# Kernel tuning notes

Hardware: AMD Instinct MI355X
Metric: run time of the kernel (lower is better)

The kernel has to match this reference:

```python
import jax, jax.numpy as jnp
import numpy as np

NUM_HEADS = 12
WINDOW = 14  # window size == input_size[0]; rel pos tables are (2*WINDOW-1, head_dim)


def setup_inputs() -> dict:
    key = jax.random.key(0)
    ks = jax.random.split(key, 6)
    C = 768
    x = jax.random.normal(ks[0], (16, 56, 56, C), dtype=jnp.float32)
    qkv_w = jax.random.normal(ks[1], (3 * C, C), dtype=jnp.float32) * 0.02
    qkv_b = jnp.zeros((3 * C,), dtype=jnp.float32)
    proj_w = jax.random.normal(ks[2], (C, C), dtype=jnp.float32) * 0.02
    proj_b = jnp.zeros((C,), dtype=jnp.float32)
    hd = C // NUM_HEADS
    rel_pos_h = jax.random.normal(ks[3], (2 * WINDOW - 1, hd), dtype=jnp.float32) * 0.02
    rel_pos_w = jax.random.normal(ks[4], (2 * WINDOW - 1, hd), dtype=jnp.float32) * 0.02
    return {"x": x, "qkv_w": qkv_w, "qkv_b": qkv_b, "proj_w": proj_w,
            "proj_b": proj_b, "rel_pos_h": rel_pos_h, "rel_pos_w": rel_pos_w}


def reference(x, qkv_w, qkv_b, proj_w, proj_b, rel_pos_h, rel_pos_w):
    B, H, W, C = x.shape
    nh, ws = NUM_HEADS, WINDOW
    hd = C // nh
    scale = hd ** -0.5
    # --- window_partition (H, W divisible by ws -> no padding branch) ---
    xw = x.reshape(B, H // ws, ws, W // ws, ws, C)
    xw = xw.transpose(0, 1, 3, 2, 4, 5).reshape(-1, ws * ws, C)  # (Bw, N, C)
    Bw, N, _ = xw.shape
    # --- qkv projection ---
    qkv = xw @ qkv_w.T + qkv_b  # (Bw, N, 3C)
    qkv = qkv.reshape(Bw, N, 3, nh, hd).transpose(2, 0, 3, 1, 4)
    qkv = qkv.reshape(3, Bw * nh, N, hd)
    q, k, v = qkv[0], qkv[1], qkv[2]
    # --- scaled attention scores ---
    attn = jnp.einsum('bqd,bkd->bqk', q * scale, k)  # (Bw*nh, N, N)
    # --- decomposed relative position bias (q_size == k_size == ws) ---
    idx = jnp.arange(ws)[:, None] - jnp.arange(ws)[None, :] + (ws - 1)
    Rh = rel_pos_h[idx]  # (ws, ws, hd)
    Rw = rel_pos_w[idx]  # (ws, ws, hd)
    rq = q.reshape(Bw * nh, ws, ws, hd)
    rel_h = jnp.einsum('bhwc,hkc->bhwk', rq, Rh)
    rel_w = jnp.einsum('bhwc,wkc->bhwk', rq, Rw)
    attn = (attn.reshape(Bw * nh, ws, ws, ws, ws)
            + rel_h[:, :, :, :, None] + rel_w[:, :, :, None, :])
    attn = jax.nn.softmax(attn.reshape(Bw * nh, N, N), axis=-1)
    # --- weighted values + output projection ---
    out = jnp.einsum('bqk,bkd->bqd', attn, v)
    out = out.reshape(Bw, nh, ws, ws, hd).transpose(0, 2, 3, 1, 4).reshape(Bw, ws, ws, C)
    out = out @ proj_w.T + proj_b
    # --- window_unpartition ---
    out = out.reshape(B, H // ws, W // ws, ws, ws, C)
    out = out.transpose(0, 1, 3, 2, 4, 5).reshape(B, H, W, C)
    return out
```

## Files before the change

kernel.cpp:

```cpp
#include <hip/hip_runtime.h>
#include <stdint.h>

typedef __bf16 bfv8 __attribute__((ext_vector_type(8)));
typedef short s16x8 __attribute__((ext_vector_type(8)));
typedef short s16x4 __attribute__((ext_vector_type(4)));
typedef float f32x4 __attribute__((ext_vector_type(4)));
typedef float f32x16 __attribute__((ext_vector_type(16)));

#define MFMA(a, b, c) __builtin_amdgcn_mfma_f32_16x16x32_bf16(a, b, c, 0, 0, 0)
#define MFMA32(a, b, c) __builtin_amdgcn_mfma_f32_32x32x16_bf16(a, b, c, 0, 0, 0)

__device__ __forceinline__ short f2bf(float f) {
  union { float f; unsigned u; } v; v.f = f;
  unsigned r = v.u + 0x7FFFu + ((v.u >> 16) & 1u);
  return (short)(r >> 16);
}
__device__ __forceinline__ float bf2f(short s) {
  union { unsigned u; float f; } v; v.u = ((unsigned)(unsigned short)s) << 16;
  return v.f;
}
__device__ __forceinline__ unsigned pack2(float a, float b) {
  return (unsigned)(unsigned short)f2bf(a) | ((unsigned)(unsigned short)f2bf(b) << 16);
}
__device__ __forceinline__ bfv8 mkfrag(unsigned a, unsigned b, unsigned c, unsigned d) {
  union { unsigned u[4]; bfv8 v; } t; t.u[0] = a; t.u[1] = b; t.u[2] = c; t.u[3] = d;
  return t.v;
}

__device__ __forceinline__ void async_cp16(const short* g, short* l) {
  auto gp = reinterpret_cast<const uint32_t __attribute__((address_space(1)))*>(
      reinterpret_cast<uintptr_t>(g));
  auto lp = reinterpret_cast<uint32_t __attribute__((address_space(3)))*>(
      reinterpret_cast<uintptr_t>(l));
  __builtin_amdgcn_global_load_lds(gp, lp, 16, 0, 0);
}

__global__ __launch_bounds__(256) void convert_all(
    const float* __restrict__ x, const float* __restrict__ qkvw,
    const float* __restrict__ projw, const float* __restrict__ rph,
    const float* __restrict__ rpw, short* __restrict__ Xbf,
    short* __restrict__ Wq, short* __restrict__ Wp, short* __restrict__ Rhb,
    short* __restrict__ Rwb) {
  const int NX = 9633792;
  const int NW1 = 442368;
  const int NW2 = 147456;
  const int NR = 512;
  int idx = blockIdx.x * 256 + threadIdx.x;
  if (idx < NX) {
    int t = idx / 192, cq = idx - t * 192;
    int wdx = t / 196, n = t - wdx * 196;
    int b = wdx >> 4, wl = wdx & 15;
    int nh = n / 14;
    int hh = (wl >> 2) * 14 + nh;
    int ww = (wl & 3) * 14 + (n - nh * 14);
    float4 v = *(const float4*)(x + ((b * 56 + hh) * 56 + ww) * 768 + cq * 4);
    s16x4 s = {f2bf(v.x), f2bf(v.y), f2bf(v.z), f2bf(v.w)};
    *(s16x4*)(Xbf + idx * 4) = s;
  } else if (idx < NX + NW1) {
    int i = idx - NX;
    float4 v = ((const float4*)qkvw)[i];
    s16x4 s = {f2bf(v.x), f2bf(v.y), f2bf(v.z), f2bf(v.w)};
    *(s16x4*)(Wq + i * 4) = s;
  } else if (idx < NX + NW1 + NW2) {
    int i = idx - NX - NW1;
    float4 v = ((const float4*)projw)[i];
    s16x4 s = {f2bf(v.x), f2bf(v.y), f2bf(v.z), f2bf(v.w)};
    *(s16x4*)(Wp + i * 4) = s;
  } else if (idx < NX + NW1 + NW2 + 2 * NR) {
    int i = idx - NX - NW1 - NW2;
    int which = i >> 9;
    int j = i & 511;
    int p = j >> 4, q = j & 15;
    const float* src = which ? rpw : rph;
    short* dst = which ? Rwb : Rhb;
    s16x4 s = {0, 0, 0, 0};
    if (p < 27) {
      float4 v = *(const float4*)(src + p * 64 + q * 4);
      s = (s16x4){f2bf(v.x), f2bf(v.y), f2bf(v.z), f2bf(v.w)};
    }
    *(s16x4*)(dst + p * 64 + q * 4) = s;
  }
}


#define GEMM_PRE()                                                            \
  const int tid = threadIdx.x, lane = tid & 63, w = tid >> 6;                 \
  const int wr = w >> 2, wc = w & 3;                                          \
  const int li = lane & 15, g = lane >> 4;                                    \
  const int lr = lane >> 3, ls = lane & 7;                                    \
  const int ss = ls ^ lr;                                                     \
  f32x4 acc[8][4];                                                            \
  _Pragma("unroll") for (int i = 0; i < 8; ++i)                               \
  _Pragma("unroll") for (int j = 0; j < 4; ++j)                               \
      acc[i][j] = (f32x4){0.f, 0.f, 0.f, 0.f};

#define GEMM_STAGE(buf, t)                                                    \
  {                                                                           \
    _Pragma("unroll") for (int q = 0; q < 4; ++q) {                           \
      async_cp16(Asrc + q * 8 * 768 + (t) * 64, &As[buf][(w * 32 + q * 8) * 64]); \
      async_cp16(Bsrc + q * 8 * 768 + (t) * 64, &Bs[buf][(w * 32 + q * 8) * 64]); \
    }                                                                         \
  }

#define GEMM_WAITBAR()                                                        \
  asm volatile("s_waitcnt vmcnt(0)" ::: "memory");                            \
  __builtin_amdgcn_sched_barrier(0);                                          \
  __builtin_amdgcn_s_barrier();

#define GEMM_COMPUTE(buf)                                                     \
  {                                                                           \
    const short* Ab = As[buf];                                                \
    const short* Bb = Bs[buf];                                                \
    bfv8 bfr[4][2];                                                           \
    _Pragma("unroll") for (int nf = 0; nf < 4; ++nf)                          \
    _Pragma("unroll") for (int kh = 0; kh < 2; ++kh)                          \
        bfr[nf][kh] = *(const bfv8*)&Bb[(wc * 64 + nf * 16 + li) * 64 +       \
                                        (((kh * 4 + g) ^ (li & 7)) * 8)];     \
    _Pragma("unroll") for (int mh = 0; mh < 2; ++mh) {                        \
      bfv8 af[4][2];                                                          \
      _Pragma("unroll") for (int mf = 0; mf < 4; ++mf)                        \
      _Pragma("unroll") for (int kh = 0; kh < 2; ++kh)                        \
          af[mf][kh] = *(const bfv8*)&Ab[(wr * 128 + mh * 64 + mf * 16 + li) * 64 + \
                                         (((kh * 4 + g) ^ (li & 7)) * 8)];    \
      __builtin_amdgcn_s_setprio(1);                                          \
      _Pragma("unroll") for (int mf = 0; mf < 4; ++mf)                        \
      _Pragma("unroll") for (int nf = 0; nf < 4; ++nf) {                      \
        acc[mh * 4 + mf][nf] = MFMA(af[mf][0], bfr[nf][0], acc[mh * 4 + mf][nf]); \
        acc[mh * 4 + mf][nf] = MFMA(af[mf][1], bfr[nf][1], acc[mh * 4 + mf][nf]); \
      }                                                                       \
      __builtin_amdgcn_s_setprio(0);                                          \
    }                                                                         \
  }

#define GEMM_LOOP()                                                           \
  GEMM_STAGE(0, 0);                                                           \
  _Pragma("unroll 1") for (int tt = 0; tt < 6; ++tt) {                        \
    GEMM_WAITBAR();                                                           \
    GEMM_STAGE(1, 2 * tt + 1);                                                \
    GEMM_COMPUTE(0);                                                          \
    GEMM_WAITBAR();                                                           \
    if (tt < 5) GEMM_STAGE(0, 2 * tt + 2);                                    \
    GEMM_COMPUTE(1);                                                          \
  }

__global__ __launch_bounds__(512, 2) void qkv_gemm(
    const short* __restrict__ Xbf, const short* __restrict__ Wq,
    const float* __restrict__ qkvb, short* __restrict__ Q,
    short* __restrict__ K, short* __restrict__ V) {
  __shared__ short As[2][256 * 64];
  __shared__ short Bs[2][256 * 64];
  int bid = blockIdx.x;
  int xcd = bid & 7, pos = bid >> 3;
  int wgid = (xcd < 4) ? xcd * 221 + pos : 884 + (xcd - 4) * 220 + pos;
  int bm = wgid / 9, bn = wgid - bm * 9;

  GEMM_PRE();
  const short* Asrc = Xbf + (bm * 256 + w * 32 + lr) * 768 + ss * 8;
  const short* Bsrc = Wq + (bn * 256 + w * 32 + lr) * 768 + ss * 8;

  GEMM_LOOP();

  short* dst = (bn < 3) ? Q : ((bn < 6) ? K : V);
  const int head = (bn % 3) * 4 + wc;
  float bias[4];
#pragma unroll
  for (int nf = 0; nf < 4; ++nf) bias[nf] = qkvb[bn * 256 + wc * 64 + nf * 16 + li];
#pragma unroll
  for (int mi = 0; mi < 8; ++mi) {
    int rbase = bm * 256 + wr * 128 + (mi >> 2) * 64 + (mi & 3) * 16 + g * 4;
#pragma unroll
    for (int j = 0; j < 4; ++j) {
      int trow = rbase + j;
      int wdx = trow / 196, n = trow - wdx * 196;
      int base = ((wdx * 12 + head) * 196 + n) * 64;
#pragma unroll
      for (int nf = 0; nf < 4; ++nf)
        dst[base + nf * 16 + li] = f2bf(acc[mi][nf][j] + bias[nf]);
    }
  }
}

__global__ __launch_bounds__(512, 2) void proj_gemm(
    const short* __restrict__ AO, const short* __restrict__ Wp,
    const float* __restrict__ projb, float* __restrict__ out) {
  __shared__ short As[2][256 * 64];
  __shared__ short Bs[2][256 * 64];
  int bid = blockIdx.x;
  int xcd = bid & 7, pos = bid >> 3;
  int wgid = (xcd < 4) ? xcd * 74 + pos : 296 + (xcd - 4) * 73 + pos;
  int bm = wgid / 3, bn = wgid - bm * 3;

  GEMM_PRE();
  const short* Asrc = AO + (bm * 256 + w * 32 + lr) * 768 + ss * 8;
  const short* Bsrc = Wp + (bn * 256 + w * 32 + lr) * 768 + ss * 8;

  GEMM_LOOP();

  float bias[4];
#pragma unroll
  for (int nf = 0; nf < 4; ++nf) bias[nf] = projb[bn * 256 + wc * 64 + nf * 16 + li];
  const int col0 = bn * 256 + wc * 64 + li;
#pragma unroll
  for (int mi = 0; mi < 8; ++mi) {
    int rbase = bm * 256 + wr * 128 + (mi >> 2) * 64 + (mi & 3) * 16 + g * 4;
#pragma unroll
    for (int j = 0; j < 4; ++j) {
      int trow = rbase + j;
      int wdx = trow / 196, n = trow - wdx * 196;
      int b = wdx >> 4, wl = wdx & 15;
      int nh = n / 14;
      int hh = (wl >> 2) * 14 + nh;
      int ww = (wl & 3) * 14 + (n - nh * 14);
      float* orow = out + ((b * 56 + hh) * 56 + ww) * 768 + col0;
#pragma unroll
      for (int nf = 0; nf < 4; ++nf)
        orow[nf * 16] = acc[mi][nf][j] + bias[nf];
    }
  }
}

__global__ __launch_bounds__(512, 4) void attn_kernel(
    const short* __restrict__ Q, const short* __restrict__ K,
    const short* __restrict__ V, const short* __restrict__ Rhb,
    const short* __restrict__ Rwb, short* __restrict__ AO) {
  __shared__ short Ks[196 * 64];
  __shared__ short Vt[64 * 204];
  __shared__ short relh[224 * 28];
  __shared__ short relw[224 * 28];
  __shared__ short2 hw[224];

  const int bh = blockIdx.x;
  const int wdx = bh / 12, head = bh - wdx * 12;
  const int tid = threadIdx.x, lane = tid & 63, wave = tid >> 6;
  const int l31 = lane & 31, hb = lane >> 5;
  const short* Qb = Q + bh * 12544;
  const short* Kb = K + bh * 12544;
  const short* Vb = V + bh * 12544;

  const int m0 = wave * 32;
  const int qv = (m0 + l31 > 195) ? 195 : m0 + l31;

  bfv8 qf[4];
  if (wave < 7) {
    f32x16 ra = {0.f, 0.f, 0.f, 0.f, 0.f, 0.f, 0.f, 0.f,
                 0.f, 0.f, 0.f, 0.f, 0.f, 0.f, 0.f, 0.f};
    f32x16 rw_ = ra;
#pragma unroll
    for (int s = 0; s < 4; ++s) {
      qf[s] = *(const bfv8*)(Qb + qv * 64 + s * 16 + hb * 8);
      ra = MFMA32(*(const bfv8*)(Rhb + l31 * 64 + s * 16 + hb * 8), qf[s], ra);
      rw_ = MFMA32(*(const bfv8*)(Rwb + l31 * 64 + s * 16 + hb * 8), qf[s], rw_);
    }
#pragma unroll
    for (int reg = 0; reg < 16; ++reg) {
      int p = (reg & 3) + 8 * (reg >> 2) + 4 * hb;
      if (!(hb && reg >= 12)) {
        relh[(m0 + l31) * 28 + p] = f2bf(ra[reg]);
        relw[(m0 + l31) * 28 + p] = f2bf(rw_[reg]);
      }
    }
  }

  if (tid < 64) {
    s16x8 z = {0, 0, 0, 0, 0, 0, 0, 0};
    *(s16x8*)&Vt[tid * 204 + 196] = z;
  }
  for (int c = tid; c < 1568; c += 512) {
    int r = c >> 3, cc = c & 7;
    s16x8 v = *(const s16x8*)(Kb + r * 64 + cc * 8);
    *(s16x8*)&Ks[r * 64 + (((cc ^ (r & 7))) << 3)] = v;
  }
  for (int t = tid; t < 784; t += 512) {
    int dseg = t / 98, kp = t - dseg * 98, d0 = dseg * 8;
    s16x8 a = *(const s16x8*)(Vb + (2 * kp) * 64 + d0);
    s16x8 b = *(const s16x8*)(Vb + (2 * kp + 1) * 64 + d0);
#pragma unroll
    for (int i = 0; i < 8; ++i)
      *(short2*)&Vt[(d0 + i) * 204 + 2 * kp] = make_short2(a[i], b[i]);
  }
  if (tid < 224) {
    int kc = (tid > 195) ? 195 : tid;
    int hk = kc / 14, wk = kc - hk * 14;
    hw[tid] = make_short2((short)(13 - hk), (short)(13 - wk));
  }
  __syncthreads();

  if (wave >= 7) return;

  const int hq = qv / 14;
  const int wq = qv - hq * 14;
  const short* relhq = &relh[qv * 28 + hq];
  const short* relwq = &relw[qv * 28 + wq];

  f32x16 oacc0 = {0.f, 0.f, 0.f, 0.f, 0.f, 0.f, 0.f, 0.f,
                  0.f, 0.f, 0.f, 0.f, 0.f, 0.f, 0.f, 0.f};
  f32x16 oacc1 = oacc0;
  float psum = 0.f;

#pragma unroll
  for (int nt = 0; nt < 7; ++nt) {
    int krow = nt * 32 + l31;
    int krc = (krow > 195) ? 195 : krow;
    const int rb = krc * 64, rx = krc & 7;
    f32x16 st = {0.f, 0.f, 0.f, 0.f, 0.f, 0.f, 0.f, 0.f,
                 0.f, 0.f, 0.f, 0.f, 0.f, 0.f, 0.f, 0.f};
#pragma unroll
    for (int s = 0; s < 4; ++s) {
      bfv8 kf = *(const bfv8*)&Ks[rb + (((2 * s + hb) ^ rx) << 3)];
      st = MFMA32(kf, qf[s], st);
    }
    float pv[16];
    float lsum = 0.f;
#pragma unroll
    for (int reg = 0; reg < 16; ++reg) {
      int koff = (reg & 3) + 8 * (reg >> 2) + 4 * hb;
      int k = nt * 32 + koff;
      short2 dxy = hw[k];
      float b = bf2f(relhq[dxy.x]) + bf2f(relwq[dxy.y]);
      float sv = fmaf(st[reg], 0.125f, b);
      float e = __expf(sv);
      if (nt == 6) {
        if (reg >= 4) e = 0.f;
        else if (hb) e = 0.f;
      }
      pv[reg] = e;
      lsum += e;
    }
    psum += lsum;
    unsigned pk[8], xk[8];
#pragma unroll
    for (int i = 0; i < 8; ++i) pk[i] = pack2(pv[2 * i], pv[2 * i + 1]);
#pragma unroll
    for (int i = 0; i < 8; ++i) xk[i] = (unsigned)__shfl_xor((int)pk[i], 32);

    {
      bfv8 pf = mkfrag(hb ? xk[2] : pk[0], hb ? xk[3] : pk[1],
                       hb ? pk[2] : xk[0], hb ? pk[3] : xk[1]);
      int kb = nt * 32 + hb * 8;
      if (nt == 6 && hb) kb = 0;
      oacc0 = MFMA32(pf, *(const bfv8*)&Vt[l31 * 204 + kb], oacc0);
      oacc1 = MFMA32(pf, *(const bfv8*)&Vt[(32 + l31) * 204 + kb], oacc1);
    }
    {
      bfv8 pf = mkfrag(hb ? xk[6] : pk[4], hb ? xk[7] : pk[5],
                       hb ? pk[6] : xk[4], hb ? pk[7] : xk[5]);
      int kb = nt * 32 + 16 + hb * 8;
      if (nt == 6) kb = 0;
      oacc0 = MFMA32(pf, *(const bfv8*)&Vt[l31 * 204 + kb], oacc0);
      oacc1 = MFMA32(pf, *(const bfv8*)&Vt[(32 + l31) * 204 + kb], oacc1);
    }
  }

  float inv = 1.f / (psum + __shfl_xor(psum, 32));
  short* AOr = AO + (wdx * 196) * 768 + head * 64;
#pragma unroll
  for (int reg = 0; reg < 16; ++reg) {
    int qoff = (reg & 3) + 8 * (reg >> 2) + 4 * hb;
    float invr = __shfl(inv, qoff);
    int q = m0 + qoff;
    if (q < 196) {
      AOr[q * 768 + l31] = f2bf(oacc0[reg] * invr);
      AOr[q * 768 + 32 + l31] = f2bf(oacc1[reg] * invr);
    }
  }
}

extern "C" void kernel_launch(void* const* d_in, const int* in_sizes, int n_in,
                              void* d_out, int out_size, void* d_ws, size_t ws_size,
                              hipStream_t stream) {
  const float* x = (const float*)d_in[0];
  const float* qkv_w = (const float*)d_in[1];
  const float* qkv_b = (const float*)d_in[2];
  const float* proj_w = (const float*)d_in[3];
  const float* proj_b = (const float*)d_in[4];
  const float* rph = (const float*)d_in[5];
  const float* rpw = (const float*)d_in[6];
  float* out = (float*)d_out;

  char* ws = (char*)d_ws;
  short* Q  = (short*)(ws);
  short* K  = (short*)(ws + 77070336);
  short* V  = (short*)(ws + 154140672);
  short* AO = (short*)(ws + 231211008);
  short* Wq = (short*)(ws + 308281344);
  short* Wp = (short*)(ws + 311820288);
  short* Xbf = (short*)d_out;
  short* Rhb = (short*)((char*)d_out + 77070336);
  short* Rwb = Rhb + 2048;

  hipLaunchKernelGGL(convert_all, dim3(39940), dim3(256), 0, stream,
                     x, qkv_w, proj_w, rph, rpw, Xbf, Wq, Wp, Rhb, Rwb);
  hipLaunchKernelGGL(qkv_gemm, dim3(1764), dim3(512), 0, stream,
                     Xbf, Wq, qkv_b, Q, K, V);
  hipLaunchKernelGGL(attn_kernel, dim3(3072), dim3(512), 0, stream,
                     Q, K, V, Rhb, Rwb, AO);
  hipLaunchKernelGGL(proj_gemm, dim3(588), dim3(512), 0, stream,
                     AO, Wp, proj_b, out);
}
```

Baseline: 461.7 us.

## Use four-stage 32-wide K pipeline with partial vmcnt waits in GEMMs

Both projection GEMMs now split K into 24 steps of 32 instead of 12 steps of 64 and cycle through four LDS buffers, keeping two loads in flight and waiting with vmcnt(4) rather than draining all memory ops every step. The loaders use a new row-per-thread layout with a matching XOR swizzle, and the LDS fragment offsets are precomputed once. The goal is to hide global-load latency behind MFMA work. In exchange there are twice as many barriers per K step and each step carries less MFMA work. LDS use stays at 128KB per block.

```diff
diff --git a/kernel.cpp b/kernel.cpp
--- a/kernel.cpp
+++ b/kernel.cpp
@@ -83,82 +83,93 @@
 }
 
 
-#define GEMM_PRE()                                                            \
+#define RPRE(ABASE, BBASE)                                                    \
   const int tid = threadIdx.x, lane = tid & 63, w = tid >> 6;                 \
   const int wr = w >> 2, wc = w & 3;                                          \
   const int li = lane & 15, g = lane >> 4;                                    \
-  const int lr = lane >> 3, ls = lane & 7;                                    \
-  const int ss = ls ^ lr;                                                     \
   f32x4 acc[8][4];                                                            \
   _Pragma("unroll") for (int i = 0; i < 8; ++i)                               \
   _Pragma("unroll") for (int j = 0; j < 4; ++j)                               \
-      acc[i][j] = (f32x4){0.f, 0.f, 0.f, 0.f};
-
-#define GEMM_STAGE(buf, t)                                                    \
+      acc[i][j] = (f32x4){0.f, 0.f, 0.f, 0.f};                                \
+  const int srow = tid >> 2;                                                  \
+  const int schunk = (lane & 3) ^ ((lane >> 3) & 3);                          \
+  const short* Asrc0 = (ABASE) + (size_t)(bm * 256 + srow) * 768 + schunk * 8;\
+  const short* Asrc1 = Asrc0 + 128 * 768;                                     \
+  const short* Bsrc0 = (BBASE) + (size_t)(bn * 256 + srow) * 768 + schunk * 8;\
+  const short* Bsrc1 = Bsrc0 + 128 * 768;                                     \
+  int aoff[2][4], boff[4];                                                    \
+  _Pragma("unroll") for (int mh = 0; mh < 2; ++mh)                            \
+  _Pragma("unroll") for (int mf = 0; mf < 4; ++mf) {                          \
+    int row = wr * 128 + mh * 64 + mf * 16 + li;                              \
+    aoff[mh][mf] = row * 64 + ((g ^ ((row >> 1) & 3)) << 4);                  \
+  }                                                                           \
+  _Pragma("unroll") for (int nf = 0; nf < 4; ++nf) {                          \
+    int row = wc * 64 + nf * 16 + li;                                         \
+    boff[nf] = 16384 + row * 64 + ((g ^ ((row >> 1) & 3)) << 4);              \
+  }
+
+#define RSTAGE(buf, t)                                                        \
   {                                                                           \
-    _Pragma("unroll") for (int q = 0; q < 4; ++q) {                           \
-      async_cp16(Asrc + q * 8 * 768 + (t) * 64, &As[buf][(w * 32 + q * 8) * 64]); \
-      async_cp16(Bsrc + q * 8 * 768 + (t) * 64, &Bs[buf][(w * 32 + q * 8) * 64]); \
-    }                                                                         \
-  }
-
-#define GEMM_WAITBAR()                                                        \
-  asm volatile("s_waitcnt vmcnt(0)" ::: "memory");                            \
-  __builtin_amdgcn_sched_barrier(0);                                          \
-  __builtin_amdgcn_s_barrier();
-
-#define GEMM_COMPUTE(buf)                                                     \
+    short* lb = LDSB + (buf) * 16384 + w * 512;                               \
+    async_cp16(Asrc0 + (t) * 32, lb);                                         \
+    async_cp16(Asrc1 + (t) * 32, lb + 4096);                                  \
+    async_cp16(Bsrc0 + (t) * 32, lb + 8192);                                  \
+    async_cp16(Bsrc1 + (t) * 32, lb + 12288);                                 \
+  }
+
+#define RCOMPUTE(buf)                                                         \
   {                                                                           \
-    const short* Ab = As[buf];                                                \
-    const short* Bb = Bs[buf];                                                \
-    bfv8 bfr[4][2];                                                           \
+    const char* bb = (const char*)LDSB + (buf) * 32768;                       \
+    bfv8 bfr[4];                                                              \
     _Pragma("unroll") for (int nf = 0; nf < 4; ++nf)                          \
-    _Pragma("unroll") for (int kh = 0; kh < 2; ++kh)                          \
-        bfr[nf][kh] = *(const bfv8*)&Bb[(wc * 64 + nf * 16 + li) * 64 +       \
-                                        (((kh * 4 + g) ^ (li & 7)) * 8)];     \
+        bfr[nf] = *(const bfv8*)(bb + boff[nf]);                              \
     _Pragma("unroll") for (int mh = 0; mh < 2; ++mh) {                        \
-      bfv8 af[4][2];                                                          \
+      bfv8 af[4];                                                             \
       _Pragma("unroll") for (int mf = 0; mf < 4; ++mf)                        \
-      _Pragma("unroll") for (int kh = 0; kh < 2; ++kh)                        \
-          af[mf][kh] = *(const bfv8*)&Ab[(wr * 128 + mh * 64 + mf * 16 + li) * 64 + \
-                                         (((kh * 4 + g) ^ (li & 7)) * 8)];    \
+          af[mf] = *(const bfv8*)(bb + aoff[mh][mf]);                         \
       __builtin_amdgcn_s_setprio(1);                                          \
       _Pragma("unroll") for (int mf = 0; mf < 4; ++mf)                        \
-      _Pragma("unroll") for (int nf = 0; nf < 4; ++nf) {                      \
-        acc[mh * 4 + mf][nf] = MFMA(af[mf][0], bfr[nf][0], acc[mh * 4 + mf][nf]); \
-        acc[mh * 4 + mf][nf] = MFMA(af[mf][1], bfr[nf][1], acc[mh * 4 + mf][nf]); \
-      }                                                                       \
+      _Pragma("unroll") for (int nf = 0; nf < 4; ++nf)                        \
+          acc[mh * 4 + mf][nf] = MFMA(af[mf], bfr[nf], acc[mh * 4 + mf][nf]); \
       __builtin_amdgcn_s_setprio(0);                                          \
     }                                                                         \
   }
 
-#define GEMM_LOOP()                                                           \
-  GEMM_STAGE(0, 0);                                                           \
-  _Pragma("unroll 1") for (int tt = 0; tt < 6; ++tt) {                        \
-    GEMM_WAITBAR();                                                           \
-    GEMM_STAGE(1, 2 * tt + 1);                                                \
-    GEMM_COMPUTE(0);                                                          \
-    GEMM_WAITBAR();                                                           \
-    if (tt < 5) GEMM_STAGE(0, 2 * tt + 2);                                    \
-    GEMM_COMPUTE(1);                                                          \
-  }
+#define RTILE(buf, t, DOSTAGE, VM)                                            \
+  asm volatile("s_waitcnt vmcnt(" VM ")" ::: "memory");                       \
+  __builtin_amdgcn_sched_barrier(0);                                          \
+  __builtin_amdgcn_s_barrier();                                               \
+  __builtin_amdgcn_sched_barrier(0);                                          \
+  if (DOSTAGE) { RSTAGE((buf + 2) & 3, (t) + 2); }                            \
+  RCOMPUTE(buf);
+
+#define RLOOP()                                                               \
+  RSTAGE(0, 0);                                                               \
+  RSTAGE(1, 1);                                                               \
+  _Pragma("unroll 1") for (int t4 = 0; t4 < 5; ++t4) {                        \
+    int tb = t4 * 4;                                                          \
+    RTILE(0, tb + 0, true, "4");                                              \
+    RTILE(1, tb + 1, true, "4");                                              \
+    RTILE(2, tb + 2, true, "4");                                              \
+    RTILE(3, tb + 3, true, "4");                                              \
+  }                                                                           \
+  RTILE(0, 20, true, "4");                                                    \
+  RTILE(1, 21, true, "4");                                                    \
+  RTILE(2, 22, false, "4");                                                   \
+  RTILE(3, 23, false, "0");
 
 __global__ __launch_bounds__(512, 2) void qkv_gemm(
     const short* __restrict__ Xbf, const short* __restrict__ Wq,
     const float* __restrict__ qkvb, short* __restrict__ Q,
     short* __restrict__ K, short* __restrict__ V) {
-  __shared__ short As[2][256 * 64];
-  __shared__ short Bs[2][256 * 64];
+  __shared__ short LDSB[65536];
   int bid = blockIdx.x;
   int xcd = bid & 7, pos = bid >> 3;
   int wgid = (xcd < 4) ? xcd * 221 + pos : 884 + (xcd - 4) * 220 + pos;
   int bm = wgid / 9, bn = wgid - bm * 9;
 
-  GEMM_PRE();
-  const short* Asrc = Xbf + (bm * 256 + w * 32 + lr) * 768 + ss * 8;
-  const short* Bsrc = Wq + (bn * 256 + w * 32 + lr) * 768 + ss * 8;
-
-  GEMM_LOOP();
+  RPRE(Xbf, Wq);
+  RLOOP();
 
   short* dst = (bn < 3) ? Q : ((bn < 6) ? K : V);
   const int head = (bn % 3) * 4 + wc;
@@ -183,18 +194,14 @@
 __global__ __launch_bounds__(512, 2) void proj_gemm(
     const short* __restrict__ AO, const short* __restrict__ Wp,
     const float* __restrict__ projb, float* __restrict__ out) {
-  __shared__ short As[2][256 * 64];
-  __shared__ short Bs[2][256 * 64];
+  __shared__ short LDSB[65536];
   int bid = blockIdx.x;
   int xcd = bid & 7, pos = bid >> 3;
   int wgid = (xcd < 4) ? xcd * 74 + pos : 296 + (xcd - 4) * 73 + pos;
   int bm = wgid / 3, bn = wgid - bm * 3;
 
-  GEMM_PRE();
-  const short* Asrc = AO + (bm * 256 + w * 32 + lr) * 768 + ss * 8;
-  const short* Bsrc = Wp + (bn * 256 + w * 32 + lr) * 768 + ss * 8;
-
-  GEMM_LOOP();
+  RPRE(AO, Wp);
+  RLOOP();
 
   float bias[4];
 #pragma unroll
```

Result: no change. 469.7 us (+1.7%).
